# Kernel tuning notes

Hardware: AMD Instinct MI355X
Metric: run time of the kernel (lower is better)

## Reference

```python
import jax, jax.numpy as jnp
import numpy as np

D_MODEL, D_HIDDEN, N_EXPERTS = 1024, 4096, 8
CAP_FACTOR, LBL_COEF, ZLOSS_COEF = 1.25, 0.01, 0.0


def setup_inputs() -> dict:
    key = jax.random.key(0)
    ks = jax.random.split(key, 4)
    B, T = 4, 2048
    x = jax.random.normal(ks[0], (B, T, D_MODEL), dtype=jnp.float32)
    # router linear
    Wr = jax.random.normal(ks[1], (D_MODEL, N_EXPERTS), jnp.float32) / np.sqrt(D_MODEL).astype(np.float32)
    br = jnp.zeros((N_EXPERTS,), jnp.float32)
    # per-expert MLP: fc1 [D->H], gelu, fc2 [H->D]
    W1 = jax.random.normal(ks[2], (N_EXPERTS, D_MODEL, D_HIDDEN), jnp.float32) / np.sqrt(D_MODEL).astype(np.float32)
    b1 = jnp.zeros((N_EXPERTS, D_HIDDEN), jnp.float32)
    W2 = jax.random.normal(ks[3], (N_EXPERTS, D_HIDDEN, D_MODEL), jnp.float32) / np.sqrt(D_HIDDEN).astype(np.float32)
    b2 = jnp.zeros((N_EXPERTS, D_MODEL), jnp.float32)
    return {"x": x, "Wr": Wr, "br": br, "W1": W1, "b1": b1, "W2": W2, "b2": b2}


def reference(x, Wr, br, W1, b1, W2, b2):
    B, T, D = x.shape
    N = B * T
    E = Wr.shape[1]
    cap = int(CAP_FACTOR * (N / E) + 1)  # static Python int

    h = x.reshape(N, D)
    # --- Top1Router ---
    logits = h @ Wr + br                              # [N, E]
    probs = jax.nn.softmax(logits, axis=-1)
    top1 = jnp.argmax(probs, axis=-1)                 # [N]
    w = jnp.take_along_axis(probs, top1[:, None], axis=1)  # [N, 1]
    assign = jax.nn.one_hot(top1, E, dtype=jnp.float32)    # constant wrt grads
    importance = probs.mean(axis=0)
    load = jax.lax.stop_gradient(assign).mean(axis=0)
    lb_loss = E * jnp.sum(importance * load)
    z_loss = jnp.mean(jax.nn.logsumexp(logits, axis=-1) ** 2)

    # --- capacity-based dispatch (first `cap` tokens per expert, token order) ---
    pos = (jnp.cumsum(assign, axis=0) * assign).sum(axis=-1).astype(jnp.int32) - 1  # [N] slot within expert
    keep = pos < cap
    slot = jnp.where(keep, pos, cap)  # dropped tokens -> overflow slot `cap`
    xe = jnp.zeros((E, cap + 1, D), x.dtype).at[top1, slot].set(h)[:, :cap]  # [E, cap, D]

    # --- per-expert MLP as grouped GEMMs ---
    he = jax.nn.gelu(jnp.einsum('ecd,edh->ech', xe, W1) + b1[:, None, :])    # [E, cap, H]
    ye = jnp.einsum('ech,ehd->ecd', he, W2) + b2[:, None, :]                 # [E, cap, D]

    # --- combine (gather back, scale by router weight, zero dropped) ---
    out = ye[top1, jnp.minimum(pos, cap - 1)] * w   # [N, D]
    out = jnp.where(keep[:, None], out, jnp.zeros((), x.dtype))
    y = out.reshape(B, T, D)
    aux = LBL_COEF * lb_loss + ZLOSS_COEF * z_loss
    return (y, aux)
```

## Files before the change

### kernel.cpp

```cpp
#include <hip/hip_runtime.h>
#include <hip/hip_bf16.h>

#define N_TOK 8192
#define DM    1024
#define DH    4096
#define NE    8
#define CAP   1281
#define CAPR  1408
#define ISTR  1536

typedef unsigned short u16;
typedef __attribute__((ext_vector_type(8))) __bf16 bf16x8;
typedef __attribute__((ext_vector_type(8))) short short8;
typedef __attribute__((ext_vector_type(4))) short s16x4;
typedef __attribute__((ext_vector_type(4))) float f4;

__device__ __forceinline__ u16 f2bf(float f){
  union { float f; unsigned u; } v; v.f = f;
  unsigned r = v.u + 0x7fffu + ((v.u >> 16) & 1u);
  return (u16)(r >> 16);
}

__device__ __forceinline__ float gelu_fast(float v){
  float u = 0.7978845608028654f * (v + 0.044715f * v * v * v);
  return v * __builtin_amdgcn_rcpf(1.0f + __expf(-2.0f * u));
}

__device__ __forceinline__ void gl2lds16(const void* g, void* l){
  __builtin_amdgcn_global_load_lds((const __attribute__((address_space(1))) void*)g,
                                   (__attribute__((address_space(3))) void*)l, 16, 0, 0);
}

__global__ __launch_bounds__(256) void tcvt_k(const float* __restrict__ W1, u16* __restrict__ W1T,
                                              const float* __restrict__ W2, u16* __restrict__ W2T){
  __shared__ float tile[64][68];
  int bid = blockIdx.x;
  int isW2 = bid >> 13;
  int local = bid & 8191;
  const float* in; u16* out; int K, Nn, bx, by, bz;
  if (!isW2){ in = W1; out = W1T; K = DM; Nn = DH; bx = local & 63; by = (local >> 6) & 15; bz = local >> 10; }
  else      { in = W2; out = W2T; K = DH; Nn = DM; bx = local & 15; by = (local >> 4) & 63; bz = local >> 10; }
  size_t mb = (size_t)bz * (size_t)K * (size_t)Nn;
  const float* ip = in + mb;
  u16* op = out + mb;
  int n0 = bx*64, k0 = by*64;
  int t = threadIdx.x;
  int kr = t>>4, nc = (t&15)*4;
  #pragma unroll
  for (int ii=0;ii<4;ii++){
    f4 v = *(const f4*)&ip[(size_t)(k0+kr+16*ii)*Nn + n0 + nc];
    tile[kr+16*ii][nc+0] = v[0]; tile[kr+16*ii][nc+1] = v[1];
    tile[kr+16*ii][nc+2] = v[2]; tile[kr+16*ii][nc+3] = v[3];
  }
  __syncthreads();
  int nr = t>>2, kc = (t&3)*16;
  short8 o0, o1;
  #pragma unroll
  for (int c=0;c<8;c++){
    o0[c] = (short)f2bf(tile[kc+c][nr]);
    o1[c] = (short)f2bf(tile[kc+8+c][nr]);
  }
  *(short8*)&op[(size_t)(n0+nr)*K + k0 + kc] = o0;
  *(short8*)&op[(size_t)(n0+nr)*K + k0 + kc + 8] = o1;
}

__global__ __launch_bounds__(256) void router_k(const float* __restrict__ x, const float* __restrict__ Wr,
    const float* __restrict__ br, u16* __restrict__ Xb, int* __restrict__ top1,
    float* __restrict__ wgt, float* __restrict__ impSum){
  __shared__ float pSh[4][8];
  int wid = threadIdx.x >> 6, lane = threadIdx.x & 63;
  int n = blockIdx.x * 4 + wid;
  const float* xr = x + (size_t)n * DM;
  u16* xbr = Xb + (size_t)n * DM;
  float acc[8];
  #pragma unroll
  for (int e=0;e<8;e++) acc[e]=0.f;
  #pragma unroll
  for (int c=0;c<4;c++){
    int d0 = c*256 + lane*4;
    f4 xv = *(const f4*)(xr + d0);
    s16x4 xb;
    #pragma unroll
    for (int j=0;j<4;j++) xb[j] = (short)f2bf(xv[j]);
    *(s16x4*)(xbr + d0) = xb;
    #pragma unroll
    for (int j=0;j<4;j++){
      const float* wrow = Wr + (size_t)(d0+j)*NE;
      float xs = xv[j];
      #pragma unroll
      for (int e=0;e<8;e++) acc[e] = fmaf(xs, wrow[e], acc[e]);
    }
  }
  #pragma unroll
  for (int off=32; off>0; off>>=1){
    #pragma unroll
    for (int e=0;e<8;e++) acc[e] += __shfl_down(acc[e], off, 64);
  }
  if (lane==0){
    float lg[8]; float mx = -1e30f;
    #pragma unroll
    for (int e=0;e<8;e++){ lg[e] = acc[e] + br[e]; mx = fmaxf(mx, lg[e]); }
    float p[8], s=0.f;
    #pragma unroll
    for (int e=0;e<8;e++){ p[e] = expf(lg[e]-mx); s += p[e]; }
    int bt=0; float bv=lg[0];
    #pragma unroll
    for (int e=1;e<8;e++){ if (lg[e]>bv){ bv=lg[e]; bt=e; } }
    float inv = 1.f/s;
    top1[n] = bt; wgt[n] = p[bt]*inv;
    #pragma unroll
    for (int e=0;e<8;e++) pSh[wid][e] = p[e]*inv;
  }
  __syncthreads();
  if (threadIdx.x < 8){
    int e = threadIdx.x;
    atomicAdd(&impSum[e], pSh[0][e]+pSh[1][e]+pSh[2][e]+pSh[3][e]);
  }
}

__global__ __launch_bounds__(1024) void scan_k(const int* __restrict__ top1, int* __restrict__ idx,
    int* __restrict__ cnt, int* __restrict__ dropList, int* __restrict__ nDrop,
    const float* __restrict__ impSum, float* __restrict__ auxOut){
  __shared__ int waveCnt[16][8];
  __shared__ int wavePre[16][8];
  __shared__ int chunkTot[8];
  __shared__ int base_s[8];
  int tid = threadIdx.x, wid = tid>>6, lane = tid&63;
  if (tid < 8) base_s[tid] = 0;
  __syncthreads();
  for (int c=0;c<8;c++){
    int t = c*1024 + tid;
    int e = top1[t];
    int myPre = 0;
    #pragma unroll
    for (int ex=0; ex<8; ex++){
      unsigned long long mk = __ballot(e == ex);
      if (lane == 0) waveCnt[wid][ex] = __popcll(mk);
      if (ex == e) myPre = __popcll(mk & ((1ull<<lane)-1ull));
    }
    __syncthreads();
    if (tid < 8){
      int run = 0;
      for (int wv=0; wv<16; wv++){ wavePre[wv][tid] = run; run += waveCnt[wv][tid]; }
      chunkTot[tid] = run;
    }
    __syncthreads();
    int pos = base_s[e] + wavePre[wid][e] + myPre;
    if (pos < CAP) idx[e*ISTR + pos] = t;
    else { int d = atomicAdd(nDrop, 1); dropList[d] = t; }
    __syncthreads();
    if (tid < 8) base_s[tid] += chunkTot[tid];
    __syncthreads();
  }
  if (tid < 8){
    cnt[tid] = base_s[tid] < CAP ? base_s[tid] : CAP;
  }
  if (tid == 0){
    float s = 0.f;
    for (int e=0;e<8;e++) s += (impSum[e]*(1.f/N_TOK)) * ((float)base_s[e]*(1.f/N_TOK));
    *auxOut = 0.01f * 8.f * s;
  }
}

__global__ __launch_bounds__(256) void zdrop_k(const int* __restrict__ dropList,
    const int* __restrict__ nDrop, float* __restrict__ y){
  int nd = *nDrop;
  for (int i = blockIdx.x; i < nd; i += gridDim.x){
    int t = dropList[i];
    f4* row = (f4*)(y + (size_t)t * DM);
    f4 z; z[0]=0.f; z[1]=0.f; z[2]=0.f; z[3]=0.f;
    row[threadIdx.x] = z;
  }
}

#define LDA(buf, m, kk) (*(const bf16x8*)&lds[(buf)*16384 + (aBase ^ ((kk)*32)) + (m)*1024])
#define LDB(buf, n, kk) (*(const bf16x8*)&lds[32768 + (buf)*16384 + (bBase ^ ((kk)*32)) + (n)*1024])

#define SA_J(buf, j, kc) gl2lds16(aS[j] + (size_t)(kc)*64, &lds[(buf)*16384 + ((j)*512 + t)*8])
#define SB_ALLM(buf, kc) do{ \
  gl2lds16(bS[0] + (size_t)(kc)*64, &lds[32768 + (buf)*16384 + (0*512 + t)*8]); \
  gl2lds16(bS[1] + (size_t)(kc)*64, &lds[32768 + (buf)*16384 + (1*512 + t)*8]); \
  gl2lds16(bS[2] + (size_t)(kc)*64, &lds[32768 + (buf)*16384 + (2*512 + t)*8]); \
  gl2lds16(bS[3] + (size_t)(kc)*64, &lds[32768 + (buf)*16384 + (3*512 + t)*8]); }while(0)

#define SB0 __builtin_amdgcn_sched_barrier(0)
#define LGKM(n) do{ asm volatile("s_waitcnt lgkmcnt(" #n ")" ::: "memory"); SB0; }while(0)

#define READ_A(dst, mbase, buf) do{ \
  dst[0][0]=LDA(buf,(mbase),0);   dst[0][1]=LDA(buf,(mbase),1); \
  dst[1][0]=LDA(buf,(mbase)+1,0); dst[1][1]=LDA(buf,(mbase)+1,1); }while(0)

#define MFMA_PAIR(q, A_) \
  _Pragma("unroll") for (int j_=0;j_<2;j_++) \
    _Pragma("unroll") for (int n_=0;n_<4;n_++) \
      _Pragma("unroll") for (int kk_=0;kk_<2;kk_++) \
        acc[2*(q)+j_][n_] = __builtin_amdgcn_mfma_f32_16x16x32_bf16(A_[j_][kk_], Bf[n_][kk_], acc[2*(q)+j_][n_], 0,0,0);

#define KTILE(buf, ktv, NTv) do{ \
  int kc1 = (ktv)+1 < (NTv) ? (ktv)+1 : (NTv)-1; \
  int kc2 = (ktv)+2 < (NTv) ? (ktv)+2 : (NTv)-1; \
  asm volatile("s_waitcnt vmcnt(6)" ::: "memory"); \
  __builtin_amdgcn_s_barrier(); \
  SA_J((buf)^1, 1, kc1); SA_J((buf)^1, 3, kc1); \
  _Pragma("unroll") for (int n_=0;n_<4;n_++){ Bf[n_][0] = LDB(buf,n_,0); Bf[n_][1] = LDB(buf,n_,1); } \
  READ_A(aA, 0, buf); \
  SB0; \
  READ_A(aB, 2, buf); \
  LGKM(4); \
  __builtin_amdgcn_s_setprio(1); MFMA_PAIR(0, aA); __builtin_amdgcn_s_setprio(0); \
  __builtin_amdgcn_s_barrier(); \
  SB_ALLM(buf, kc2); \
  READ_A(aA, 4, buf); \
  LGKM(4); \
  __builtin_amdgcn_s_setprio(1); MFMA_PAIR(1, aB); __builtin_amdgcn_s_setprio(0); \
  __builtin_amdgcn_s_barrier(); \
  SA_J(buf, 0, kc2); SA_J(buf, 2, kc2); \
  READ_A(aB, 6, buf); \
  LGKM(4); \
  __builtin_amdgcn_s_setprio(1); MFMA_PAIR(2, aA); __builtin_amdgcn_s_setprio(0); \
  __builtin_amdgcn_s_barrier(); \
  LGKM(0); \
  __builtin_amdgcn_s_setprio(1); MFMA_PAIR(3, aB); __builtin_amdgcn_s_setprio(0); \
}while(0)

#define GEMM_PROLOGUE() do{ \
  SB_ALLM(0, 0); \
  SA_J(0,0,0); SA_J(0,2,0); \
  SA_J(0,1,0); SA_J(0,3,0); \
  SB_ALLM(1, 1); \
  SA_J(1,0,1); SA_J(1,2,1); }while(0)

__global__ __launch_bounds__(512, 2) void gemm1_k(
    const u16* __restrict__ Xb, const u16* __restrict__ W1T,
    const float* __restrict__ b1, const int* __restrict__ idx,
    const int* __restrict__ cnt, u16* __restrict__ He)
{
  int bid = blockIdx.x;
  int x = bid & 7, k = bid >> 3;
  int g = x*16 + k/6;
  int ntS = k - (k/6)*6;
  int e = g >> 4, mtH = g & 15;
  int cn = cnt[e];
  if (ntS*256 >= cn) return;
  __shared__ __align__(16) u16 lds[65536];
  int t = threadIdx.x, lane = t&63, wid = t>>6;
  int waveM = wid>>2, waveN = wid&3;
  int rA = lane&15, kb = lane>>4, s = rA&7;

  const u16* aS[4]; const u16* bS[4];
  #pragma unroll
  for (int j=0;j<4;j++){
    int pos = j*512 + t;
    int row = pos>>3, ch = pos&7;
    int gcb = ch ^ (row&7);
    aS[j] = W1T + ((size_t)e*DH + mtH*256 + row)*DM + gcb*8;
    int slotrow = ntS*256 + row;
    int token = (slotrow < cn) ? idx[e*ISTR + slotrow] : 0;
    bS[j] = Xb + (size_t)token*DM + gcb*8;
  }
  f4 acc[8][4];
  #pragma unroll
  for (int m=0;m<8;m++)
    #pragma unroll
    for (int n=0;n<4;n++)
      #pragma unroll
      for (int j=0;j<4;j++) acc[m][n][j]=0.f;

  int aBase = (waveM*128 + rA)*64 + (kb ^ s)*8;
  int bBase = (waveN*64  + rA)*64 + (kb ^ s)*8;
  bf16x8 Bf[4][2], aA[2][2], aB[2][2];

  GEMM_PROLOGUE();
  const int NT = DM/64;
  #pragma unroll 1
  for (int i=0;i<NT/2;i++){
    KTILE(0, 2*i,   NT);
    KTILE(1, 2*i+1, NT);
  }
  asm volatile("s_waitcnt vmcnt(0) lgkmcnt(0)" ::: "memory");

  int rG = lane>>4;
  #pragma unroll
  for (int m=0;m<8;m++){
    int h0 = mtH*256 + waveM*128 + m*16 + rG*4;
    f4 b4 = *(const f4*)&b1[e*DH + h0];
    #pragma unroll
    for (int n=0;n<4;n++){
      int slot = ntS*256 + waveN*64 + n*16 + rA;
      if (slot < cn){
        s16x4 v;
        #pragma unroll
        for (int j=0;j<4;j++) v[j] = (short)f2bf(gelu_fast(acc[m][n][j] + b4[j]));
        *(s16x4*)&He[((size_t)e*CAPR + slot)*DH + h0] = v;
      }
    }
  }
}

__global__ __launch_bounds__(512, 2) void gemm2_k(
    const u16* __restrict__ He, const u16* __restrict__ W2T,
    const float* __restrict__ b2, const int* __restrict__ idx,
    const int* __restrict__ cnt, const float* __restrict__ wgt,
    float* __restrict__ y)
{
  int bid = blockIdx.x;
  int x = bid & 7, k = bid >> 3;
  int g = x*4 + k/6;
  int mt = k - (k/6)*6;
  int e = g >> 2, nt = g & 3;
  int cn = cnt[e];
  if (mt*256 >= cn) return;
  __shared__ __align__(16) u16 lds[65536];
  int t = threadIdx.x, lane = t&63, wid = t>>6;
  int waveM = wid>>2, waveN = wid&3;
  int rA = lane&15, kb = lane>>4, s = rA&7;

  const u16* aS[4]; const u16* bS[4];
  #pragma unroll
  for (int j=0;j<4;j++){
    int pos = j*512 + t;
    int row = pos>>3, ch = pos&7;
    int gcb = ch ^ (row&7);
    int srow = mt*256 + row; if (srow >= cn) srow = cn-1;
    aS[j] = He  + ((size_t)e*CAPR + srow)*DH + gcb*8;
    bS[j] = W2T + ((size_t)e*DM + nt*256 + row)*DH + gcb*8;
  }
  f4 acc[8][4];
  #pragma unroll
  for (int m=0;m<8;m++)
    #pragma unroll
    for (int n=0;n<4;n++)
      #pragma unroll
      for (int j=0;j<4;j++) acc[m][n][j]=0.f;

  int aBase = (waveM*128 + rA)*64 + (kb ^ s)*8;
  int bBase = (waveN*64  + rA)*64 + (kb ^ s)*8;
  bf16x8 Bf[4][2], aA[2][2], aB[2][2];

  GEMM_PROLOGUE();
  const int NT = DH/64;
  #pragma unroll 1
  for (int i=0;i<NT/2;i++){
    KTILE(0, 2*i,   NT);
    KTILE(1, 2*i+1, NT);
  }
  asm volatile("s_waitcnt vmcnt(0) lgkmcnt(0)" ::: "memory");

  int rG = lane>>4;
  float bias_[4];
  #pragma unroll
  for (int n=0;n<4;n++) bias_[n] = b2[e*DM + nt*256 + waveN*64 + n*16 + rA];
  #pragma unroll
  for (int m=0;m<8;m++){
    int slot0 = mt*256 + waveM*128 + m*16 + rG*4;
    #pragma unroll
    for (int j=0;j<4;j++){
      int slot = slot0 + j;
      bool valid = slot < cn;
      int tk = valid ? idx[e*ISTR + slot] : 0;
      float wv = valid ? wgt[tk] : 0.f;
      float* yr = y + (size_t)tk*DM;
      #pragma unroll
      for (int n=0;n<4;n++){
        int col = nt*256 + waveN*64 + n*16 + rA;
        if (valid) yr[col] = (acc[m][n][j] + bias_[n]) * wv;
      }
    }
  }
}

extern "C" void kernel_launch(void* const* d_in, const int* in_sizes, int n_in,
                              void* d_out, int out_size, void* d_ws, size_t ws_size,
                              hipStream_t stream){
  const float* x  = (const float*)d_in[0];
  const float* Wr = (const float*)d_in[1];
  const float* br = (const float*)d_in[2];
  const float* W1 = (const float*)d_in[3];
  const float* b1 = (const float*)d_in[4];
  const float* W2 = (const float*)d_in[5];
  const float* b2 = (const float*)d_in[6];
  float* y = (float*)d_out;

  char* ws = (char*)d_ws;
  u16* Xb  = (u16*)(ws);
  u16* W1T = (u16*)(ws + 16777216ull);
  u16* W2T = (u16*)(ws + 16777216ull + 67108864ull);
  u16* He  = (u16*)(ws + 16777216ull + 2ull*67108864ull);
  char* tail = ws + 16777216ull + 2ull*67108864ull + (size_t)NE*CAPR*DH*2ull;
  int*   top1   = (int*)(tail);
  float* wgt    = (float*)(tail + 32768);
  int*   idx    = (int*)(tail + 65536);
  int*   drop   = (int*)(tail + 65536 + 49152);
  float* impSum = (float*)(tail + 65536 + 49152 + 32768);
  int*   nDrop  = (int*)((char*)impSum + 32);
  int*   cnt    = nDrop + 1;

  (void)hipMemsetAsync(impSum, 0, 64, stream);

  tcvt_k<<<16384, 256, 0, stream>>>(W1, W1T, W2, W2T);
  router_k<<<2048, 256, 0, stream>>>(x, Wr, br, Xb, top1, wgt, impSum);
  scan_k<<<1, 1024, 0, stream>>>(top1, idx, cnt, drop, nDrop, impSum,
                                 y + (size_t)N_TOK*DM);
  zdrop_k<<<64, 256, 0, stream>>>(drop, nDrop, y);
  gemm1_k<<<768, 512, 0, stream>>>(Xb, W1T, b1, idx, cnt, He);
  gemm2_k<<<192, 512, 0, stream>>>(He, W2T, b2, idx, cnt, wgt, y);

  (void)in_sizes; (void)n_in; (void)out_size; (void)ws_size;
}
```

Baseline: 342.5 us.

## Overlap W2 transpose-convert with gemm1 by appending extra blocks

Splits the weight transpose/convert kernel so only W1 is converted up front. The W2 conversion moves into extra trailing blocks of the gemm1 launch, two 256-thread tiles per 512-thread block, so the memory-bound conversion can fill idle CUs alongside the compute-bound GEMM. The tile padding also changes from 68 to 65 floats to reduce LDS bank conflicts. The conversion blocks carry gemm1's 512-thread launch and its large LDS allocation, which may limit how many run at once and could interfere with the GEMM blocks.

```diff
diff --git a/kernel.cpp b/kernel.cpp
--- a/kernel.cpp
+++ b/kernel.cpp
@@ -31,37 +31,33 @@
                                    (__attribute__((address_space(3))) void*)l, 16, 0, 0);
 }
 
-__global__ __launch_bounds__(256) void tcvt_k(const float* __restrict__ W1, u16* __restrict__ W1T,
-                                              const float* __restrict__ W2, u16* __restrict__ W2T){
-  __shared__ float tile[64][68];
-  int bid = blockIdx.x;
-  int isW2 = bid >> 13;
-  int local = bid & 8191;
-  const float* in; u16* out; int K, Nn, bx, by, bz;
-  if (!isW2){ in = W1; out = W1T; K = DM; Nn = DH; bx = local & 63; by = (local >> 6) & 15; bz = local >> 10; }
-  else      { in = W2; out = W2T; K = DH; Nn = DM; bx = local & 15; by = (local >> 4) & 63; bz = local >> 10; }
-  size_t mb = (size_t)bz * (size_t)K * (size_t)Nn;
-  const float* ip = in + mb;
-  u16* op = out + mb;
-  int n0 = bx*64, k0 = by*64;
-  int t = threadIdx.x;
-  int kr = t>>4, nc = (t&15)*4;
+__device__ __forceinline__ void tcvt_tile(const float* __restrict__ ip, u16* __restrict__ op,
+                                          int K, int Nn, int n0, int k0, int tt, float* tile){
+  int kr = tt>>4, nc = (tt&15)*4;
   #pragma unroll
   for (int ii=0;ii<4;ii++){
     f4 v = *(const f4*)&ip[(size_t)(k0+kr+16*ii)*Nn + n0 + nc];
-    tile[kr+16*ii][nc+0] = v[0]; tile[kr+16*ii][nc+1] = v[1];
-    tile[kr+16*ii][nc+2] = v[2]; tile[kr+16*ii][nc+3] = v[3];
+    float* row = &tile[(kr+16*ii)*65 + nc];
+    row[0]=v[0]; row[1]=v[1]; row[2]=v[2]; row[3]=v[3];
   }
   __syncthreads();
-  int nr = t>>2, kc = (t&3)*16;
+  int nr = tt>>2, kc = (tt&3)*16;
   short8 o0, o1;
   #pragma unroll
   for (int c=0;c<8;c++){
-    o0[c] = (short)f2bf(tile[kc+c][nr]);
-    o1[c] = (short)f2bf(tile[kc+8+c][nr]);
+    o0[c] = (short)f2bf(tile[(kc+c)*65 + nr]);
+    o1[c] = (short)f2bf(tile[(kc+8+c)*65 + nr]);
   }
   *(short8*)&op[(size_t)(n0+nr)*K + k0 + kc] = o0;
   *(short8*)&op[(size_t)(n0+nr)*K + k0 + kc + 8] = o1;
+}
+
+__global__ __launch_bounds__(256) void tcvt1_k(const float* __restrict__ W1, u16* __restrict__ W1T){
+  __shared__ float tile[64*65];
+  int local = blockIdx.x;
+  int bx = local & 63, by = (local >> 6) & 15, bz = local >> 10;
+  size_t mb = (size_t)bz * (size_t)DM * (size_t)DH;
+  tcvt_tile(W1 + mb, W1T + mb, DM, DH, bx*64, by*64, threadIdx.x, tile);
 }
 
 __global__ __launch_bounds__(256) void router_k(const float* __restrict__ x, const float* __restrict__ Wr,
@@ -233,17 +229,28 @@
 __global__ __launch_bounds__(512, 2) void gemm1_k(
     const u16* __restrict__ Xb, const u16* __restrict__ W1T,
     const float* __restrict__ b1, const int* __restrict__ idx,
-    const int* __restrict__ cnt, u16* __restrict__ He)
+    const int* __restrict__ cnt, u16* __restrict__ He,
+    const float* __restrict__ W2, u16* __restrict__ W2T)
 {
+  __shared__ __align__(16) u16 lds[65536];
   int bid = blockIdx.x;
+  int t = threadIdx.x;
+  if (bid >= 768){
+    int half = t >> 8, tt = t & 255;
+    int tau = (bid - 768)*2 + half;
+    int bx = tau & 15, by = (tau >> 4) & 63, bz = tau >> 10;
+    size_t mb = (size_t)bz * (size_t)DH * (size_t)DM;
+    float* tile = ((float*)lds) + half*4160;
+    tcvt_tile(W2 + mb, W2T + mb, DH, DM, bx*64, by*64, tt, tile);
+    return;
+  }
   int x = bid & 7, k = bid >> 3;
   int g = x*16 + k/6;
   int ntS = k - (k/6)*6;
   int e = g >> 4, mtH = g & 15;
   int cn = cnt[e];
   if (ntS*256 >= cn) return;
-  __shared__ __align__(16) u16 lds[65536];
-  int t = threadIdx.x, lane = t&63, wid = t>>6;
+  int lane = t&63, wid = t>>6;
   int waveM = wid>>2, waveN = wid&3;
   int rA = lane&15, kb = lane>>4, s = rA&7;
 
@@ -397,12 +404,12 @@
 
   (void)hipMemsetAsync(impSum, 0, 64, stream);
 
-  tcvt_k<<<16384, 256, 0, stream>>>(W1, W1T, W2, W2T);
+  tcvt1_k<<<8192, 256, 0, stream>>>(W1, W1T);
   router_k<<<2048, 256, 0, stream>>>(x, Wr, br, Xb, top1, wgt, impSum);
   scan_k<<<1, 1024, 0, stream>>>(top1, idx, cnt, drop, nDrop, impSum,
                                  y + (size_t)N_TOK*DM);
   zdrop_k<<<64, 256, 0, stream>>>(drop, nDrop, y);
-  gemm1_k<<<768, 512, 0, stream>>>(Xb, W1T, b1, idx, cnt, He);
+  gemm1_k<<<768 + 4096, 512, 0, stream>>>(Xb, W1T, b1, idx, cnt, He, W2, W2T);
   gemm2_k<<<192, 512, 0, stream>>>(He, W2T, b2, idx, cnt, wgt, y);
 
   (void)in_sizes; (void)n_in; (void)out_size; (void)ws_size;
```

Result: no change. 339.8 us (-0.8%).
